# Optimization experiments

Hardware: AMD Instinct MI355X
Metric: run time of the kernel (lower is better)

The kernel has to match this reference:

```python
import jax, jax.numpy as jnp
import numpy as np


def _build_sparse_conv_problem():
    # Mirrors torchsparse rulebook construction for Conv3d(1,16,k=3,stride=2).
    rng = np.random.default_rng(0)
    B, R, N, Cin, Cout, S = 2, 512, 2_000_000, 1, 16, 2
    vol = R * R * R
    keys = np.unique(rng.integers(0, B * vol, size=int(N * 1.25), dtype=np.int64))[:N]
    b = keys // vol
    rem = keys % vol
    x = rem // (R * R)
    y = (rem // R) % R
    z = rem % R
    # output coords: unique floor-division by stride (torchsparse downsample)
    Ro = R // S
    ovol = Ro * Ro * Ro
    okeys = np.unique(((b * Ro + x // S) * Ro + (y // S)) * Ro + (z // S))
    n_out = int(okeys.shape[0])
    ob = okeys // ovol
    orem = okeys % ovol
    ox = orem // (Ro * Ro)
    oy = (orem // Ro) % Ro
    oz = orem % Ro
    # rulebook: for each of 27 offsets, find inputs at out*stride + offset
    in_list, out_list, k_list = [], [], []
    k = 0
    for dx in (-1, 0, 1):
        for dy in (-1, 0, 1):
            for dz in (-1, 0, 1):
                qx = ox * S + dx
                qy = oy * S + dy
                qz = oz * S + dz
                valid = (qx >= 0) & (qx < R) & (qy >= 0) & (qy < R) & (qz >= 0) & (qz < R)
                qkey = ((ob * R + qx) * R + qy) * R + qz
                pos = np.searchsorted(keys, qkey)
                pos = np.clip(pos, 0, N - 1)
                hit = valid & (keys[pos] == qkey)
                in_list.append(pos[hit].astype(np.int32))
                out_list.append(np.nonzero(hit)[0].astype(np.int32))
                k_list.append(np.full(int(hit.sum()), k, np.int32))
                k += 1
    in_idx = np.concatenate(in_list)
    out_idx = np.concatenate(out_list)
    k_idx = np.concatenate(k_list)
    return N, Cin, Cout, n_out, in_idx, out_idx, k_idx


def setup_inputs() -> dict:
    N, Cin, Cout, n_out, in_idx, out_idx, k_idx = _build_sparse_conv_problem()
    kf, kw = jax.random.split(jax.random.key(0))
    feats = jax.random.normal(kf, (N, Cin), dtype=jnp.float32)          # x.F
    weight = jax.random.normal(kw, (27, Cin, Cout), dtype=jnp.float32) * 0.1  # conv1 kernel
    return {
        "feats": feats,
        "weight": weight,
        "in_idx": jnp.asarray(in_idx),
        "out_idx": jnp.asarray(out_idx),
        "k_idx": jnp.asarray(k_idx),
        "n_out": n_out,
    }


def reference(feats, weight, in_idx, out_idx, k_idx, n_out):
    # gather-GEMM-scatter sparse 3D conv: out[o] += W[k] @ feats[i] for each
    # rulebook pair (i, o, k).
    gathered = feats[in_idx]                       # [M, Cin]
    contrib = jnp.einsum('mc,mco->mo', gathered, weight[k_idx])  # [M, Cout]
    return jax.ops.segment_sum(contrib, out_idx, num_segments=n_out)  # [n_out, Cout]
```

## Files before the change

kernel.cpp:

```cpp
#include <hip/hip_runtime.h>


typedef float vf4 __attribute__((ext_vector_type(4)));
typedef int   vi4 __attribute__((ext_vector_type(4)));

__device__ inline unsigned short f32_to_bf16_rne(float x) {
    unsigned int u = __float_as_uint(x);
    unsigned int r = 0x7FFFu + ((u >> 16) & 1u);
    return (unsigned short)((u + r) >> 16);
}

__device__ inline int dense_plane(int k) {
    int a = k / 9, b = (k / 3) % 3, c = k % 3;
    if (a == 0 || b == 0 || c == 0) return -1;
    return ((a - 1) << 2) | ((b - 1) << 1) | (c - 1);
}

__global__ void __launch_bounds__(256)
scatter_dense4(const float* __restrict__ feats,
               const int* __restrict__ in_idx,
               const int* __restrict__ out_idx,
               const int* __restrict__ k_idx,
               unsigned short* __restrict__ g,
               int M, int np) {
    int t = blockIdx.x * blockDim.x + threadIdx.x;
    int base = t * 4;
    if (base + 3 < M) {
        vi4 kk = *(const vi4*)&k_idx[base];
        vi4 ii = *(const vi4*)&in_idx[base];
        vi4 oo = *(const vi4*)&out_idx[base];
        int p0 = dense_plane(kk.x), p1 = dense_plane(kk.y),
            p2 = dense_plane(kk.z), p3 = dense_plane(kk.w);
        float f0 = feats[ii.x], f1 = feats[ii.y],
              f2 = feats[ii.z], f3 = feats[ii.w];
        if (p0 >= 0) g[(size_t)p0 * np + oo.x] = f32_to_bf16_rne(f0);
        if (p1 >= 0) g[(size_t)p1 * np + oo.y] = f32_to_bf16_rne(f1);
        if (p2 >= 0) g[(size_t)p2 * np + oo.z] = f32_to_bf16_rne(f2);
        if (p3 >= 0) g[(size_t)p3 * np + oo.w] = f32_to_bf16_rne(f3);
    } else if (base < M) {
        for (int m = base; m < M; ++m) {
            int p = dense_plane(k_idx[m]);
            if (p >= 0)
                g[(size_t)p * np + out_idx[m]] =
                    f32_to_bf16_rne(feats[in_idx[m]]);
        }
    }
}

__global__ void __launch_bounds__(256, 4)
reduce8(const unsigned int* __restrict__ g32,
        const float* __restrict__ weight,
        float* __restrict__ out,
        int n_out, int half_np) {
    int t = blockIdx.x * blockDim.x + threadIdx.x;
    int o0 = t * 2;
    if (o0 >= n_out) return;

    unsigned int gu[8];
    #pragma unroll
    for (int p = 0; p < 8; ++p)
        gu[p] = g32[(size_t)p * half_np + t];

    vf4 a0 = {0,0,0,0}, a1 = a0, a2 = a0, a3 = a0;
    vf4 b0 = a0, b1 = a0, b2 = a0, b3 = a0;
    const int KP[8] = {13, 14, 16, 17, 22, 23, 25, 26};
    #pragma unroll
    for (int p = 0; p < 8; ++p) {
        const vf4* w = (const vf4*)&weight[KP[p] * 16];
        vf4 w0 = w[0], w1 = w[1], w2 = w[2], w3 = w[3];
        float fa = __uint_as_float(gu[p] << 16);
        float fb = __uint_as_float(gu[p] & 0xFFFF0000u);
        a0 += fa * w0; a1 += fa * w1; a2 += fa * w2; a3 += fa * w3;
        b0 += fb * w0; b1 += fb * w1; b2 += fb * w2; b3 += fb * w3;
    }

    vf4* op = (vf4*)(out + (size_t)o0 * 16);
    op[0] = a0; op[1] = a1; op[2] = a2; op[3] = a3;
    if (o0 + 1 < n_out) {
        op[4] = b0; op[5] = b1; op[6] = b2; op[7] = b3;
    }
}

__global__ void __launch_bounds__(256)
sparse_scan_add4(const float* __restrict__ feats,
                 const float* __restrict__ weight,
                 const int* __restrict__ in_idx,
                 const int* __restrict__ out_idx,
                 const int* __restrict__ k_idx,
                 float* __restrict__ out,
                 int M) {
    long long t = (long long)blockIdx.x * blockDim.x + threadIdx.x;
    int grp = (int)(t >> 4);
    int c   = (int)(t & 15);
    int base = grp * 4;
    if (base >= M) return;
    if (base + 3 < M) {
        vi4 kk = *(const vi4*)&k_idx[base];
        int p0 = dense_plane(kk.x), p1 = dense_plane(kk.y),
            p2 = dense_plane(kk.z), p3 = dense_plane(kk.w);
        if ((p0 | p1 | p2 | p3) >= 0) return;
        vi4 ii = *(const vi4*)&in_idx[base];
        vi4 oo = *(const vi4*)&out_idx[base];
        if (p0 < 0) {
            float f = feats[ii.x];
            atomicAdd(out + (long long)oo.x * 16 + c, f * weight[kk.x * 16 + c]);
        }
        if (p1 < 0) {
            float f = feats[ii.y];
            atomicAdd(out + (long long)oo.y * 16 + c, f * weight[kk.y * 16 + c]);
        }
        if (p2 < 0) {
            float f = feats[ii.z];
            atomicAdd(out + (long long)oo.z * 16 + c, f * weight[kk.z * 16 + c]);
        }
        if (p3 < 0) {
            float f = feats[ii.w];
            atomicAdd(out + (long long)oo.w * 16 + c, f * weight[kk.w * 16 + c]);
        }
    } else {
        for (int m = base; m < M; ++m) {
            int k = k_idx[m];
            if (dense_plane(k) >= 0) continue;
            float f = feats[in_idx[m]];
            atomicAdd(out + (long long)out_idx[m] * 16 + c,
                      f * weight[k * 16 + c]);
        }
    }
}

__global__ void __launch_bounds__(256)
sparse_conv_scatter_atomic(const float* __restrict__ feats,
                           const float* __restrict__ weight,
                           const int* __restrict__ in_idx,
                           const int* __restrict__ out_idx,
                           const int* __restrict__ k_idx,
                           float* __restrict__ out,
                           int M) {
    long long t = (long long)blockIdx.x * blockDim.x + threadIdx.x;
    int m = (int)(t >> 4);
    int c = (int)(t & 15);
    if (m >= M) return;
    float f = feats[in_idx[m]];
    float w = weight[k_idx[m] * 16 + c];
    atomicAdd(out + (long long)out_idx[m] * 16 + c, f * w);
}

extern "C" void kernel_launch(void* const* d_in, const int* in_sizes, int n_in,
                              void* d_out, int out_size, void* d_ws, size_t ws_size,
                              hipStream_t stream) {
    const float* feats  = (const float*)d_in[0];
    const float* weight = (const float*)d_in[1];
    const int*   in_idx = (const int*)d_in[2];
    const int*   out_idx= (const int*)d_in[3];
    const int*   k_idx  = (const int*)d_in[4];
    float*       out    = (float*)d_out;

    const int M     = in_sizes[2];
    const int n_out = out_size / 16;
    const int np    = (n_out + 1) & ~1;

    const size_t need = (size_t)8 * (size_t)np * sizeof(unsigned short);
    const int block = 256;

    if (d_ws != nullptr && ws_size >= need) {
        unsigned short* g = (unsigned short*)d_ws;
        hipMemsetAsync(g, 0, need, stream);

        const int nthr1 = (M + 3) / 4;
        const int grid1 = (nthr1 + block - 1) / block;
        scatter_dense4<<<grid1, block, 0, stream>>>(feats, in_idx, out_idx,
                                                    k_idx, g, M, np);

        const int nthr2 = (n_out + 1) / 2;
        const int grid2 = (nthr2 + block - 1) / block;
        reduce8<<<grid2, block, 0, stream>>>((const unsigned int*)g, weight,
                                             out, n_out, np / 2);

        const long long nthr3 = (long long)((M + 3) / 4) * 16;
        const int grid3 = (int)((nthr3 + block - 1) / block);
        sparse_scan_add4<<<grid3, block, 0, stream>>>(feats, weight, in_idx,
                                                      out_idx, k_idx, out, M);
    } else {
        hipMemsetAsync(d_out, 0, (size_t)out_size * sizeof(float), stream);
        const long long total = (long long)M * 16;
        const long long grid = (total + block - 1) / block;
        sparse_conv_scatter_atomic<<<(int)grid, block, 0, stream>>>(
            feats, weight, in_idx, out_idx, k_idx, out, M);
    }
}
```

Baseline: 243.0 us.

## Fuse sparse atomic pass into dense scatter via shared-memory compaction list

The separate sparse_scan_add4 kernel, which re-read the whole rulebook to handle non-dense offsets, is removed. The scatter kernel now records non-dense rulebook entries in a shared-memory list and processes them with 16-lane atomicAdds into out, which is zeroed up front. reduce8 then accumulates into out with read-modify-write instead of plain stores. This avoids a second full pass over the index arrays, at the cost of an extra memset of the output, an extra output read in reduce8, and shared-memory atomics with an irregular tail loop.

New measurement: 292.9 us. 20.5% more time.

```diff
diff --git a/kernel.cpp b/kernel.cpp
--- a/kernel.cpp
+++ b/kernel.cpp
@@ -17,12 +17,19 @@
 }
 
 __global__ void __launch_bounds__(256)
-scatter_dense4(const float* __restrict__ feats,
-               const int* __restrict__ in_idx,
-               const int* __restrict__ out_idx,
-               const int* __restrict__ k_idx,
-               unsigned short* __restrict__ g,
-               int M, int np) {
+fused_scatter(const float* __restrict__ feats,
+              const float* __restrict__ weight,
+              const int* __restrict__ in_idx,
+              const int* __restrict__ out_idx,
+              const int* __restrict__ k_idx,
+              unsigned short* __restrict__ g,
+              float* __restrict__ out,
+              int M, int np) {
+    __shared__ int sl[1024];
+    __shared__ int sc;
+    if (threadIdx.x == 0) sc = 0;
+    __syncthreads();
+
     int t = blockIdx.x * blockDim.x + threadIdx.x;
     int base = t * 4;
     if (base + 3 < M) {
@@ -34,16 +41,34 @@
         float f0 = feats[ii.x], f1 = feats[ii.y],
               f2 = feats[ii.z], f3 = feats[ii.w];
         if (p0 >= 0) g[(size_t)p0 * np + oo.x] = f32_to_bf16_rne(f0);
+        else         sl[atomicAdd(&sc, 1)] = base + 0;
         if (p1 >= 0) g[(size_t)p1 * np + oo.y] = f32_to_bf16_rne(f1);
+        else         sl[atomicAdd(&sc, 1)] = base + 1;
         if (p2 >= 0) g[(size_t)p2 * np + oo.z] = f32_to_bf16_rne(f2);
+        else         sl[atomicAdd(&sc, 1)] = base + 2;
         if (p3 >= 0) g[(size_t)p3 * np + oo.w] = f32_to_bf16_rne(f3);
+        else         sl[atomicAdd(&sc, 1)] = base + 3;
     } else if (base < M) {
         for (int m = base; m < M; ++m) {
             int p = dense_plane(k_idx[m]);
             if (p >= 0)
                 g[(size_t)p * np + out_idx[m]] =
                     f32_to_bf16_rne(feats[in_idx[m]]);
+            else
+                sl[atomicAdd(&sc, 1)] = m;
         }
+    }
+    __syncthreads();
+
+    int nsp = sc;
+    int grp = threadIdx.x >> 4;
+    int c   = threadIdx.x & 15;
+    for (int e = grp; e < nsp; e += 16) {
+        int m = sl[e];
+        int k = k_idx[m];
+        float f = feats[in_idx[m]];
+        atomicAdd(out + (long long)out_idx[m] * 16 + c,
+                  f * weight[k * 16 + c]);
     }
 }
 
@@ -75,56 +100,9 @@
     }
 
     vf4* op = (vf4*)(out + (size_t)o0 * 16);
-    op[0] = a0; op[1] = a1; op[2] = a2; op[3] = a3;
+    op[0] += a0; op[1] += a1; op[2] += a2; op[3] += a3;
     if (o0 + 1 < n_out) {
-        op[4] = b0; op[5] = b1; op[6] = b2; op[7] = b3;
-    }
-}
-
-__global__ void __launch_bounds__(256)
-sparse_scan_add4(const float* __restrict__ feats,
-                 const float* __restrict__ weight,
-                 const int* __restrict__ in_idx,
-                 const int* __restrict__ out_idx,
-                 const int* __restrict__ k_idx,
-                 float* __restrict__ out,
-                 int M) {
-    long long t = (long long)blockIdx.x * blockDim.x + threadIdx.x;
-    int grp = (int)(t >> 4);
-    int c   = (int)(t & 15);
-    int base = grp * 4;
-    if (base >= M) return;
-    if (base + 3 < M) {
-        vi4 kk = *(const vi4*)&k_idx[base];
-        int p0 = dense_plane(kk.x), p1 = dense_plane(kk.y),
-            p2 = dense_plane(kk.z), p3 = dense_plane(kk.w);
-        if ((p0 | p1 | p2 | p3) >= 0) return;
-        vi4 ii = *(const vi4*)&in_idx[base];
-        vi4 oo = *(const vi4*)&out_idx[base];
-        if (p0 < 0) {
-            float f = feats[ii.x];
-            atomicAdd(out + (long long)oo.x * 16 + c, f * weight[kk.x * 16 + c]);
-        }
-        if (p1 < 0) {
-            float f = feats[ii.y];
-            atomicAdd(out + (long long)oo.y * 16 + c, f * weight[kk.y * 16 + c]);
-        }
-        if (p2 < 0) {
-            float f = feats[ii.z];
-            atomicAdd(out + (long long)oo.z * 16 + c, f * weight[kk.z * 16 + c]);
-        }
-        if (p3 < 0) {
-            float f = feats[ii.w];
-            atomicAdd(out + (long long)oo.w * 16 + c, f * weight[kk.w * 16 + c]);
-        }
-    } else {
-        for (int m = base; m < M; ++m) {
-            int k = k_idx[m];
-            if (dense_plane(k) >= 0) continue;
-            float f = feats[in_idx[m]];
-            atomicAdd(out + (long long)out_idx[m] * 16 + c,
-                      f * weight[k * 16 + c]);
-        }
+        op[4] += b0; op[5] += b1; op[6] += b2; op[7] += b3;
     }
 }
 
@@ -165,21 +143,18 @@
     if (d_ws != nullptr && ws_size >= need) {
         unsigned short* g = (unsigned short*)d_ws;
         hipMemsetAsync(g, 0, need, stream);
+        hipMemsetAsync(out, 0, (size_t)out_size * sizeof(float), stream);
 
         const int nthr1 = (M + 3) / 4;
         const int grid1 = (nthr1 + block - 1) / block;
-        scatter_dense4<<<grid1, block, 0, stream>>>(feats, in_idx, out_idx,
-                                                    k_idx, g, M, np);
+        fused_scatter<<<grid1, block, 0, stream>>>(feats, weight, in_idx,
+                                                   out_idx, k_idx, g, out,
+                                                   M, np);
 
         const int nthr2 = (n_out + 1) / 2;
         const int grid2 = (nthr2 + block - 1) / block;
         reduce8<<<grid2, block, 0, stream>>>((const unsigned int*)g, weight,
                                              out, n_out, np / 2);
-
-        const long long nthr3 = (long long)((M + 3) / 4) * 16;
-        const int grid3 = (int)((nthr3 + block - 1) / block);
-        sparse_scan_add4<<<grid3, block, 0, stream>>>(feats, weight, in_idx,
-                                                      out_idx, k_idx, out, M);
     } else {
         hipMemsetAsync(d_out, 0, (size_t)out_size * sizeof(float), stream);
         const long long total = (long long)M * 16;
```
